# Kernel tuning notes

Measured on AMD Instinct MI355X. Metric: run time of the kernel, lower is better.

Reference implementation:

```python
import jax, jax.numpy as jnp
import numpy as np

SPLIT = [0, 4096, 5120, 5376, 5440, 5456, 5460]
FMAPS = [64, 32, 16, 8, 4, 2]
N_CAND = 9
ALPHA_REG = 1.0
FL_ALPHA, FL_GAMMA = 0.25, 2.0
N_CLASSES = 81
B, O = 64, 16


def make_priors():
    ps = []
    for fm in FMAPS:
        c = (np.arange(fm, dtype=np.float32) + 0.5) / fm
        cy, cx = np.meshgrid(c, c, indexing='ij')
        wh = np.full_like(cx, 1.5 / fm)
        ps.append(np.stack([cx.ravel(), cy.ravel(), wh.ravel(), wh.ravel()], 1))
    return jnp.asarray(np.concatenate(ps, 0))


def cxcy_to_xy(b):
    return jnp.concatenate([b[..., :2] - b[..., 2:] / 2, b[..., :2] + b[..., 2:] / 2], -1)


def xy_to_cxcy(b):
    return jnp.concatenate([(b[..., :2] + b[..., 2:]) / 2, b[..., 2:] - b[..., :2]], -1)


def decode(g, p):  # gcxgcy_to_cxcy, SSD-style variances (10, 5)
    return jnp.concatenate([g[:, :2] * p[:, 2:] / 10 + p[:, :2], jnp.exp(g[:, 2:] / 5) * p[:, 2:]], 1)


def iou_matrix(a, b):  # a [N,4], b [M,4], corner format -> [N,M]
    tl = jnp.maximum(a[:, None, :2], b[None, :, :2])
    br = jnp.minimum(a[:, None, 2:], b[None, :, 2:])
    inter = jnp.clip(br - tl, 0.0).prod(-1)
    area_a = (a[:, 2:] - a[:, :2]).prod(-1)
    area_b = (b[:, 2:] - b[:, :2]).prod(-1)
    return inter / (area_a[:, None] + area_b[None, :] - inter + 1e-10)


def assign_one(p_locs, boxes_xy, labels_i, priors):
    """ATSS assignment for one image. p_locs [P,4], boxes_xy [O,4], labels_i [O]."""
    boxes_cxcy = xy_to_cxcy(boxes_xy)
    tops, povs = [], []
    for l in range(6):
        pl = priors[SPLIT[l]:SPLIT[l + 1]]
        k = min(N_CAND, pl.shape[0])
        dist = jnp.linalg.norm(boxes_cxcy[:, None, :2] - pl[None, :, :2], axis=-1)  # [O,P_l]
        _, ti = jax.lax.top_k(-dist, k)  # k nearest priors per object
        ov = iou_matrix(boxes_xy, cxcy_to_xy(pl))
        tops.append(ti)
        povs.append(jnp.take_along_axis(ov, ti, axis=1))  # [O,k]
    pov_cat = jnp.concatenate(povs, 1)  # [O,49]
    thresh = pov_cat.mean(1) + jnp.std(pov_cat, axis=1, ddof=1)  # torch.std unbiased
    n_obj = boxes_xy.shape[0]
    labels_all, pred_all, tgt_all, mask_all = [], [], [], []
    for l in range(6):
        pl = priors[SPLIT[l]:SPLIT[l + 1]]
        ti, pov = tops[l], povs[l]
        cand = pl[ti]  # [O,k,4] candidate prior cxcywh
        inside = ((boxes_xy[:, None, 0] <= cand[..., 0]) & (cand[..., 0] <= boxes_xy[:, None, 2]) &
                  (boxes_xy[:, None, 1] <= cand[..., 1]) & (cand[..., 1] <= boxes_xy[:, None, 3]))
        pos = (pov > thresh[:, None]) & inside  # [O,k]
        ob_ids = jnp.broadcast_to(jnp.arange(n_obj, dtype=jnp.int32)[:, None], pos.shape)
        winner = jnp.full((pl.shape[0],), -1, jnp.int32).at[ti.ravel()].max(
            jnp.where(pos, ob_ids, -1).ravel())
        labels_all.append(jnp.where(winner >= 0, labels_i[jnp.clip(winner, 0)], 0))
        dec = cxcy_to_xy(decode(p_locs[SPLIT[l]:SPLIT[l + 1]], pl))  # [P_l,4]
        pred_all.append(dec[ti].reshape(-1, 4))
        tgt_all.append(jnp.broadcast_to(boxes_xy[:, None, :], cand.shape).reshape(-1, 4))
        mask_all.append(pos.ravel())
    return (jnp.concatenate(labels_all), jnp.concatenate(pred_all),
            jnp.concatenate(tgt_all), jnp.concatenate(mask_all))


def diou_loss(pred, tgt):  # corner boxes [N,4] -> [N]
    tl = jnp.maximum(pred[:, :2], tgt[:, :2])
    br = jnp.minimum(pred[:, 2:], tgt[:, 2:])
    inter = jnp.clip(br - tl, 0.0).prod(-1)
    ap = jnp.clip(pred[:, 2:] - pred[:, :2], 0.0).prod(-1)
    at = (tgt[:, 2:] - tgt[:, :2]).prod(-1)
    iou = inter / (ap + at - inter + 1e-7)
    cp = (pred[:, :2] + pred[:, 2:]) / 2
    ct = (tgt[:, :2] + tgt[:, 2:]) / 2
    d2 = ((cp - ct) ** 2).sum(-1)
    etl = jnp.minimum(pred[:, :2], tgt[:, :2])
    ebr = jnp.maximum(pred[:, 2:], tgt[:, 2:])
    diag2 = ((ebr - etl) ** 2).sum(-1) + 1e-7
    return 1.0 - iou + d2 / diag2


def focal(scores, targets):  # sigmoid focal loss, summed
    t = jax.nn.one_hot(targets, scores.shape[1], dtype=scores.dtype)
    p = jax.nn.sigmoid(scores)
    ce = -(t * jax.nn.log_sigmoid(scores) + (1 - t) * jax.nn.log_sigmoid(-scores))
    w = jnp.where(t > 0, FL_ALPHA * (1 - p) ** FL_GAMMA, (1 - FL_ALPHA) * p ** FL_GAMMA)
    return (w * ce).sum()


def setup_inputs() -> dict:
    key = jax.random.key(0)
    k1, k2, k3, k4, k5 = jax.random.split(key, 5)
    predicted_locs = jax.random.normal(k1, (B, SPLIT[-1], 4), jnp.float32)
    predicted_scores = jax.random.normal(k2, (B, SPLIT[-1], N_CLASSES), jnp.float32)
    ctr = jax.random.uniform(k3, (B, O, 2), jnp.float32, 0.25, 0.75)
    wh = jax.random.uniform(k4, (B, O, 2), jnp.float32, 0.08, 0.4)
    boxes = jnp.clip(jnp.concatenate([ctr - wh / 2, ctr + wh / 2], -1), 0.0, 1.0)
    labels = jax.random.randint(k5, (B, O), 1, N_CLASSES, jnp.int32)
    return {"predicted_locs": predicted_locs, "predicted_scores": predicted_scores,
            "boxes": boxes, "labels": labels, "priors_cxcy": make_priors()}


def reference(predicted_locs, predicted_scores, boxes, labels, priors_cxcy):
    assign = jax.vmap(assign_one, in_axes=(0, 0, 0, None))
    true_cls, pred_boxes, tgt_boxes, pos_mask = assign(predicted_locs, boxes, labels, priors_cxcy)
    true_cls = true_cls.reshape(-1)  # [B*5460]
    scores = predicted_scores.reshape(-1, predicted_scores.shape[-1])
    conf_loss = focal(scores, true_cls) / true_cls.shape[0]
    pb = pred_boxes.reshape(-1, 4)
    tb = tgt_boxes.reshape(-1, 4)
    m = pos_mask.reshape(-1).astype(pb.dtype)
    loc_loss = (diou_loss(pb, tb) * m).sum() / jnp.maximum(m.sum(), 1.0)
    return conf_loss + ALPHA_REG * loc_loss
```

## Files before the change

kernel.cpp:

```cpp
#include <hip/hip_runtime.h>
#include <float.h>
#include <limits.h>

#define NB 64
#define NO 16
#define NP 5460
#define NCLS 81

#define WS_ACCUM   0
#define WS_WINNER  256
#define WS_CI      1398272
#define WS_OV      1660672

__global__ __launch_bounds__(256) void topk_kernel(
    const float* __restrict__ boxes,
    int* __restrict__ ci_buf,
    float* __restrict__ ov_buf)
{
    const int tid = blockIdx.x * 256 + threadIdx.x;
    const int l  = tid >> 10;
    const int bo = tid & 1023;

    const int fms[6]   = {64, 32, 16, 8, 4, 2};
    const int lg2s[6]  = {6, 5, 4, 3, 2, 1};
    const int s0s[6]   = {0, 4096, 5120, 5376, 5440, 5456};
    const int basec[6] = {0, 9, 18, 27, 36, 45};
    const int fm = fms[l];
    const int lg2 = lg2s[l];
    const float fmf = (float)fm;

    const float4 bb = reinterpret_cast<const float4*>(boxes)[bo];
    const float bx0 = bb.x, by0 = bb.y, bx1 = bb.z, by1 = bb.w;
    const float bcx = (bx0 + bx1) * 0.5f;
    const float bcy = (by0 + by1) * 0.5f;
    const float barea = (bx1 - bx0) * (by1 - by0);

    int wx0 = 0, wy0 = 0, wnx = fm, wny = fm;
    if (fm >= 5) {
        int jx = (int)floorf(bcx * fmf);
        int jy = (int)floorf(bcy * fmf);
        jx = jx < 0 ? 0 : (jx > fm - 1 ? fm - 1 : jx);
        jy = jy < 0 ? 0 : (jy > fm - 1 ? fm - 1 : jy);
        wx0 = jx - 2; wx0 = wx0 < 0 ? 0 : (wx0 > fm - 5 ? fm - 5 : wx0);
        wy0 = jy - 2; wy0 = wy0 < 0 ? 0 : (wy0 > fm - 5 ? fm - 5 : wy0);
        wnx = 5; wny = 5;
    }

    float bv[9]; int bix[9];
    #pragma unroll
    for (int j = 0; j < 9; ++j) { bv[j] = FLT_MAX; bix[j] = INT_MAX; }

    for (int yy = 0; yy < wny; ++yy) {
        const int iy = wy0 + yy;
        const float py = ((float)iy + 0.5f) / fmf;
        const float dy = bcy - py;
        const float dy2 = dy * dy;
        for (int xx = 0; xx < wnx; ++xx) {
            const int ix = wx0 + xx;
            const float px = ((float)ix + 0.5f) / fmf;
            const float dx = bcx - px;
            const float d = dx * dx + dy2;
            const int gi = (iy << lg2) + ix;
            #pragma unroll
            for (int j = 8; j >= 0; --j) {
                bool ltp = (j > 0) ? (d < bv[j - 1]) : false;
                bool ltj = (d < bv[j]);
                float sv = ltp ? bv[j - 1] : (ltj ? d : bv[j]);
                int   si = ltp ? bix[j - 1] : (ltj ? gi : bix[j]);
                bv[j] = sv; bix[j] = si;
            }
        }
    }

    const int n = fm * fm;
    const int k = n < 9 ? n : 9;
    const float hw = 0.75f / fmf;
    const int obase = bo * 64 + basec[l];
    const int s0 = s0s[l];

    for (int j = 0; j < k; ++j) {
        const int li = bix[j];
        const int iy = li >> lg2, ix = li & (fm - 1);
        const float pcx = ((float)ix + 0.5f) / fmf;
        const float pcy = ((float)iy + 0.5f) / fmf;
        const float px0 = pcx - hw, py0 = pcy - hw;
        const float px1 = pcx + hw, py1 = pcy + hw;
        const float iw = fmaxf(fminf(bx1, px1) - fmaxf(bx0, px0), 0.f);
        const float ih = fmaxf(fminf(by1, py1) - fmaxf(by0, py0), 0.f);
        const float inter = iw * ih;
        const float parea = (px1 - px0) * (py1 - py0);
        const float ovv = inter / (barea + parea - inter + 1e-10f);
        ci_buf[obase + j] = s0 + li;
        ov_buf[obase + j] = ovv;
    }
}

__global__ __launch_bounds__(256) void assign2_kernel(
    const float* __restrict__ locs,
    const float* __restrict__ boxes,
    const float* __restrict__ priors,
    const int* __restrict__ ci_buf,
    const float* __restrict__ ov_buf,
    int* __restrict__ winner,
    double* __restrict__ accum)
{
    const int w = threadIdx.x >> 6, lane = threadIdx.x & 63;
    const int bo = blockIdx.x * 4 + w;
    const int b = bo >> 4, o = bo & 15;

    const float4 bb = reinterpret_cast<const float4*>(boxes)[bo];
    const float bx0 = bb.x, by0 = bb.y, bx1 = bb.z, by1 = bb.w;
    const float bcx = (bx0 + bx1) * 0.5f, bcy = (by0 + by1) * 0.5f;
    const float barea = (bx1 - bx0) * (by1 - by0);

    int my_ci = 0; float ov = 0.f;
    if (lane < 49) {
        my_ci = ci_buf[bo * 64 + lane];
        ov    = ov_buf[bo * 64 + lane];
    }

    float sum = 0.f;
    for (int i = 0; i < 49; ++i) sum += __shfl(ov, i);
    const float mean = sum / 49.f;
    float ss = 0.f;
    for (int i = 0; i < 49; ++i) { float dd = __shfl(ov, i) - mean; ss += dd * dd; }
    const float thr = mean + sqrtf(ss / 48.f);

    float lloc = 0.f; int lcnt = 0;
    if (lane < 49) {
        const float4 pp = reinterpret_cast<const float4*>(priors)[my_ci];
        const bool inside = (bx0 <= pp.x) && (pp.x <= bx1) &&
                            (by0 <= pp.y) && (pp.y <= by1);
        if (inside && ov > thr) {
            atomicMax(&winner[b * NP + my_ci], o);
            const float4 g = reinterpret_cast<const float4*>(locs)[b * NP + my_ci];
            const float cx = g.x * pp.z * 0.1f + pp.x;
            const float cy = g.y * pp.w * 0.1f + pp.y;
            const float ww = __expf(g.z * 0.2f) * pp.z;
            const float hh = __expf(g.w * 0.2f) * pp.w;
            const float p0 = cx - ww * 0.5f, p1 = cy - hh * 0.5f;
            const float p2 = cx + ww * 0.5f, p3 = cy + hh * 0.5f;
            const float iw = fmaxf(fminf(p2, bx1) - fmaxf(p0, bx0), 0.f);
            const float ih = fmaxf(fminf(p3, by1) - fmaxf(p1, by0), 0.f);
            const float inter = iw * ih;
            const float ap = fmaxf(p2 - p0, 0.f) * fmaxf(p3 - p1, 0.f);
            const float iou = inter / (ap + barea - inter + 1e-7f);
            const float cpx = (p0 + p2) * 0.5f, cpy = (p1 + p3) * 0.5f;
            const float d2 = (cpx - bcx) * (cpx - bcx) + (cpy - bcy) * (cpy - bcy);
            const float ex0 = fminf(p0, bx0), ey0 = fminf(p1, by0);
            const float ex1 = fmaxf(p2, bx1), ey1 = fmaxf(p3, by1);
            const float dg = (ex1 - ex0) * (ex1 - ex0) + (ey1 - ey0) * (ey1 - ey0) + 1e-7f;
            lloc = 1.f - iou + d2 / dg;
            lcnt = 1;
        }
    }
    #pragma unroll
    for (int off = 32; off > 0; off >>= 1) {
        lloc += __shfl_xor(lloc, off);
        lcnt += __shfl_xor(lcnt, off);
    }
    if (lane == 0 && lcnt > 0) {
        atomicAdd(&accum[1], (double)lloc);
        atomicAdd(&accum[2], (double)lcnt);
    }
}

__global__ __launch_bounds__(256) void focal_kernel(
    const float* __restrict__ scores,
    const int* __restrict__ winner,
    const int* __restrict__ labels,
    double* __restrict__ accum)
{
    const unsigned total4 = (unsigned)(NB * NP * NCLS / 4);
    const float4* s4 = reinterpret_cast<const float4*>(scores);
    float lsum = 0.f;
    for (unsigned i = blockIdx.x * blockDim.x + threadIdx.x; i < total4;
         i += gridDim.x * blockDim.x) {
        float4 v = s4[i];
        unsigned base = i * 4u;
        unsigned row = base / 81u;
        int c = (int)(base - row * 81u);
        int w = winner[row];
        int L = (w >= 0) ? labels[(row / NP) * NO + w] : 0;
        float vv[4] = {v.x, v.y, v.z, v.w};
        #pragma unroll
        for (int j = 0; j < 4; ++j) {
            if (c == 81) {
                c = 0; ++row;
                int w2 = winner[row];
                L = (w2 >= 0) ? labels[(row / NP) * NO + w2] : 0;
            }
            float s = vv[j];
            float e = __expf(-fabsf(s));
            float l1p = __logf(1.f + e);
            float q = __frcp_rn(1.f + e);
            float p   = (s >= 0.f) ? q : e * q;
            float omp = (s >= 0.f) ? e * q : q;
            float val;
            if (c == L) {
                val = 0.25f * omp * omp * (fmaxf(-s, 0.f) + l1p);
            } else {
                val = 0.75f * p * p * (fmaxf(s, 0.f) + l1p);
            }
            lsum += val;
            ++c;
        }
    }
    __shared__ float red[4];
    #pragma unroll
    for (int off = 32; off > 0; off >>= 1) lsum += __shfl_xor(lsum, off);
    int wid = threadIdx.x >> 6, lane = threadIdx.x & 63;
    if (lane == 0) red[wid] = lsum;
    __syncthreads();
    if (threadIdx.x == 0) {
        float t = red[0] + red[1] + red[2] + red[3];
        atomicAdd(&accum[0], (double)t);
    }
}

__global__ void finalize_kernel(const double* __restrict__ accum,
                                float* __restrict__ out)
{
    double conf = accum[0] / (double)(NB * NP);
    double cnt = accum[2];
    double loc = accum[1] / (cnt > 1.0 ? cnt : 1.0);
    out[0] = (float)(conf + loc);
}

extern "C" void kernel_launch(void* const* d_in, const int* in_sizes, int n_in,
                              void* d_out, int out_size, void* d_ws, size_t ws_size,
                              hipStream_t stream) {
    const float* locs   = (const float*)d_in[0];
    const float* scores = (const float*)d_in[1];
    const float* boxes  = (const float*)d_in[2];
    const int*   labels = (const int*)d_in[3];
    const float* priors = (const float*)d_in[4];
    float* out = (float*)d_out;

    double* accum = (double*)((char*)d_ws + WS_ACCUM);
    int*    winner = (int*)((char*)d_ws + WS_WINNER);
    int*    ci_buf = (int*)((char*)d_ws + WS_CI);
    float*  ov_buf = (float*)((char*)d_ws + WS_OV);

    hipMemsetAsync((char*)d_ws + WS_ACCUM, 0, 64, stream);
    hipMemsetAsync(winner, 0xFF, (size_t)NB * NP * sizeof(int), stream);

    topk_kernel<<<24, 256, 0, stream>>>(boxes, ci_buf, ov_buf);
    assign2_kernel<<<256, 256, 0, stream>>>(locs, boxes, priors, ci_buf, ov_buf,
                                            winner, accum);
    focal_kernel<<<2048, 256, 0, stream>>>(scores, winner, labels, accum);
    finalize_kernel<<<1, 1, 0, stream>>>(accum, out);
}
```

Baseline: 240.9 us.

## Split focal loss into uniform negative sum plus per-row positive-class correction

The focal kernel now treats every score as a negative, which removes the per-element row/class index arithmetic (division by 81), the winner and label lookups and the branch. A new fixup kernel then gathers one score per prior row at its assigned label and adds the positive-minus-negative difference in double. This decouples the streaming pass from the assignment output. The cost is an extra kernel launch, a scattered gather over the score tensor, and slight rounding differences from subtracting terms.

```diff
diff --git a/kernel.cpp b/kernel.cpp
--- a/kernel.cpp
+++ b/kernel.cpp
@@ -11,6 +11,21 @@
 #define WS_WINNER  256
 #define WS_CI      1398272
 #define WS_OV      1660672
+
+__device__ __forceinline__ float focal_neg(float s) {
+    float e = __expf(-fabsf(s));
+    float l1p = __logf(1.f + e);
+    float q = __frcp_rn(1.f + e);
+    float p = (s >= 0.f) ? q : e * q;
+    return 0.75f * p * p * (fmaxf(s, 0.f) + l1p);
+}
+__device__ __forceinline__ float focal_pos(float s) {
+    float e = __expf(-fabsf(s));
+    float l1p = __logf(1.f + e);
+    float q = __frcp_rn(1.f + e);
+    float omp = (s >= 0.f) ? e * q : q;
+    return 0.25f * omp * omp * (fmaxf(-s, 0.f) + l1p);
+}
 
 __global__ __launch_bounds__(256) void topk_kernel(
     const float* __restrict__ boxes,
@@ -165,10 +180,8 @@
     }
 }
 
-__global__ __launch_bounds__(256) void focal_kernel(
+__global__ __launch_bounds__(256) void focal_neg_kernel(
     const float* __restrict__ scores,
-    const int* __restrict__ winner,
-    const int* __restrict__ labels,
     double* __restrict__ accum)
 {
     const unsigned total4 = (unsigned)(NB * NP * NCLS / 4);
@@ -177,34 +190,10 @@
     for (unsigned i = blockIdx.x * blockDim.x + threadIdx.x; i < total4;
          i += gridDim.x * blockDim.x) {
         float4 v = s4[i];
-        unsigned base = i * 4u;
-        unsigned row = base / 81u;
-        int c = (int)(base - row * 81u);
-        int w = winner[row];
-        int L = (w >= 0) ? labels[(row / NP) * NO + w] : 0;
-        float vv[4] = {v.x, v.y, v.z, v.w};
-        #pragma unroll
-        for (int j = 0; j < 4; ++j) {
-            if (c == 81) {
-                c = 0; ++row;
-                int w2 = winner[row];
-                L = (w2 >= 0) ? labels[(row / NP) * NO + w2] : 0;
-            }
-            float s = vv[j];
-            float e = __expf(-fabsf(s));
-            float l1p = __logf(1.f + e);
-            float q = __frcp_rn(1.f + e);
-            float p   = (s >= 0.f) ? q : e * q;
-            float omp = (s >= 0.f) ? e * q : q;
-            float val;
-            if (c == L) {
-                val = 0.25f * omp * omp * (fmaxf(-s, 0.f) + l1p);
-            } else {
-                val = 0.75f * p * p * (fmaxf(s, 0.f) + l1p);
-            }
-            lsum += val;
-            ++c;
-        }
+        lsum += focal_neg(v.x);
+        lsum += focal_neg(v.y);
+        lsum += focal_neg(v.z);
+        lsum += focal_neg(v.w);
     }
     __shared__ float red[4];
     #pragma unroll
@@ -215,6 +204,29 @@
     if (threadIdx.x == 0) {
         float t = red[0] + red[1] + red[2] + red[3];
         atomicAdd(&accum[0], (double)t);
+    }
+}
+
+__global__ __launch_bounds__(256) void fixup_kernel(
+    const float* __restrict__ scores,
+    const int* __restrict__ winner,
+    const int* __restrict__ labels,
+    double* __restrict__ accum)
+{
+    const int r = blockIdx.x * 256 + threadIdx.x;
+    const int w = winner[r];
+    const int L = (w >= 0) ? labels[(r / NP) * NO + w] : 0;
+    const float s = scores[r * NCLS + L];
+    double d = (double)focal_pos(s) - (double)focal_neg(s);
+
+    __shared__ double redd[4];
+    #pragma unroll
+    for (int off = 32; off > 0; off >>= 1) d += __shfl_xor(d, off);
+    int wid = threadIdx.x >> 6, lane = threadIdx.x & 63;
+    if (lane == 0) redd[wid] = d;
+    __syncthreads();
+    if (threadIdx.x == 0) {
+        atomicAdd(&accum[0], redd[0] + redd[1] + redd[2] + redd[3]);
     }
 }
 
@@ -248,6 +260,7 @@
     topk_kernel<<<24, 256, 0, stream>>>(boxes, ci_buf, ov_buf);
     assign2_kernel<<<256, 256, 0, stream>>>(locs, boxes, priors, ci_buf, ov_buf,
                                             winner, accum);
-    focal_kernel<<<2048, 256, 0, stream>>>(scores, winner, labels, accum);
+    focal_neg_kernel<<<2048, 256, 0, stream>>>(scores, accum);
+    fixup_kernel<<<NB * NP / 256, 256, 0, stream>>>(scores, winner, labels, accum);
     finalize_kernel<<<1, 1, 0, stream>>>(accum, out);
 }
```

After: 256.4 us. 6.4% more time.
